# Performance work log

Measured on AMD Instinct MI355X. Metric: run time of the kernel, lower is better.

The kernel has to match this reference:

```python
import jax, jax.numpy as jnp
import numpy as np
from jax import lax

N_CHANNELS = 64
N_FILTERS = 256
N_LAYERS = 9  # residual blocks use dilations 2**1 .. 2**(N_LAYERS-1)


def causal_conv1d(x, w, dilation):
    """Causal dilated conv. x: [B,T,Cin], w: [K,Cin,Cout]."""
    pad = (w.shape[0] - 1) * dilation
    return lax.conv_general_dilated(
        x, w, window_strides=(1,), padding=[(pad, 0)],
        rhs_dilation=(dilation,), dimension_numbers=("NWC", "WIO", "NWC"))


def setup_inputs() -> dict:
    key = jax.random.key(0)
    ks = jax.random.split(key, 12)
    B, T, C, F, L = 8, 4096, N_CHANNELS, N_FILTERS, N_LAYERS
    s = lambda fan_in: 1.0 / np.sqrt(fan_in)
    return {
        "x": jax.random.normal(ks[0], (B, T, C), jnp.float32),
        "Wc": jax.random.normal(ks[1], (2, C, F), jnp.float32) * s(2 * C),
        "Wf": jax.random.normal(ks[2], (L - 1, 2, F, F), jnp.float32) * s(2 * F),
        "Wg": jax.random.normal(ks[3], (L - 1, 2, F, F), jnp.float32) * s(2 * F),
        "Wr": jax.random.normal(ks[4], (L - 1, F, F), jnp.float32) * s(F),
        "br": jnp.zeros((L - 1, F), jnp.float32),
        "Ws": jax.random.normal(ks[5], (L - 1, F, F), jnp.float32) * s(F),
        "bs": jnp.zeros((L - 1, F), jnp.float32),
        "Wd1": jax.random.normal(ks[6], (F, C), jnp.float32) * s(F),
        "bd1": jnp.zeros((C,), jnp.float32),
        "Wd2": jax.random.normal(ks[7], (C, C), jnp.float32) * s(C),
        "bd2": jnp.zeros((C,), jnp.float32),
    }


def reference(x, Wc, Wf, Wg, Wr, br, Ws, bs, Wd1, bd1, Wd2, bd2):
    # Initial causal conv, dilation 1, no bias.
    out = causal_conv1d(x, Wc, 1)  # [B,T,F]
    skip_sum = jnp.zeros_like(out)
    for i in range(N_LAYERS - 1):
        d = 2 ** (i + 1)
        f = causal_conv1d(out, Wf[i], d)
        g = causal_conv1d(out, Wg[i], d)
        z = jnp.tanh(f) * jax.nn.sigmoid(g)
        out = out + jnp.einsum("btf,fo->bto", z, Wr[i]) + br[i]
        skip_sum = skip_sum + jnp.einsum("btf,fo->bto", z, Ws[i]) + bs[i]
    h = jax.nn.selu(skip_sum)
    h = jnp.einsum("btf,fc->btc", h, Wd1) + bd1
    h = jax.nn.selu(h)
    h = jnp.einsum("btc,co->bto", h, Wd2) + bd2
    return h
```

## Files before the change

### kernel.cpp

```cpp
#include <hip/hip_runtime.h>
#include <cstdint>

typedef unsigned short u16;
typedef unsigned int u32;
typedef __attribute__((ext_vector_type(8))) short s8v;
typedef __attribute__((ext_vector_type(4))) float f4v;

#define FCH 256

__device__ __forceinline__ float bf2f(u16 u){ return __uint_as_float(((u32)u)<<16); }
__device__ __forceinline__ u16 f2bf(float x){
  u32 u = __float_as_uint(x);
  u += 0x7fffu + ((u>>16)&1u);
  return (u16)(u>>16);
}
__device__ __forceinline__ float rcpf(float x){ return __builtin_amdgcn_rcpf(x); }
__device__ __forceinline__ uint4 pack8(float4 a, float4 b){
  uint4 o;
  o.x = (u32)f2bf(a.x) | ((u32)f2bf(a.y)<<16);
  o.y = (u32)f2bf(a.z) | ((u32)f2bf(a.w)<<16);
  o.z = (u32)f2bf(b.x) | ((u32)f2bf(b.y)<<16);
  o.w = (u32)f2bf(b.z) | ((u32)f2bf(b.w)<<16);
  return o;
}
__device__ __forceinline__ float seluf(float x){
  const float sc = 1.0507009873554805f, al = 1.6732632423543772f;
  return x > 0.f ? sc*x : sc*al*(__expf(x)-1.f);
}
__device__ __forceinline__ s8v ldmask(const u16* p, u32 m){
  uint4 r = *reinterpret_cast<const uint4*>(p);
  r.x &= m; r.y &= m; r.z &= m; r.w &= m;
  s8v v; *reinterpret_cast<uint4*>(&v) = r;
  return v;
}
__device__ __forceinline__ int xcd_tile(int bid, int nT8){
  return nT8 ? ((bid & 7) * nT8 + (bid >> 3)) : bid;
}

__global__ __launch_bounds__(256) void pack_kernel(
    const float* __restrict__ Wc, const float* __restrict__ Wf, const float* __restrict__ Wg,
    const float* __restrict__ Wr, const float* __restrict__ Ws,
    const float* __restrict__ Wd1, const float* __restrict__ Wd2,
    u16* __restrict__ Bp1, u16* __restrict__ Bp2, u16* __restrict__ Bp0,
    u16* __restrict__ BpD1, u16* __restrict__ BpD2)
{
  int gid = blockIdx.x*256 + threadIdx.x;
  int frag = gid >> 6;
  int lane = gid & 63;
  int q = lane >> 4, i15 = lane & 15;
  u16 v[8];
  u16* dst;
  if (frag < 4096) {
    int layer = frag >> 9, rem = frag & 511;
    int kc = rem >> 5, nt = rem & 31;
    int n = nt*16 + i15;
    const float* W = (n < 256) ? Wf : Wg;
    int nn = (n < 256) ? n : n - 256;
    #pragma unroll
    for (int j = 0; j < 8; ++j) {
      int k = kc*32 + q*8 + j;
      int tap = k >> 8, cin = k & 255;
      v[j] = f2bf(W[((size_t)((layer*2 + tap)*256 + cin))*256 + nn]);
    }
    dst = Bp1 + (size_t)frag*512 + lane*8;
  } else if (frag < 6144) {
    int f = frag - 4096;
    int layer = f >> 8, rem = f & 255;
    int kc = rem >> 5, nt = rem & 31;
    int n = nt*16 + i15;
    const float* W = (n < 256) ? Wr : Ws;
    int nn = (n < 256) ? n : n - 256;
    #pragma unroll
    for (int j = 0; j < 8; ++j) {
      int k = kc*32 + q*8 + j;
      v[j] = f2bf(W[((size_t)(layer*256 + k))*256 + nn]);
    }
    dst = Bp2 + (size_t)f*512 + lane*8;
  } else if (frag < 6208) {
    int f = frag - 6144;
    int kc = f >> 4, nt = f & 15;
    int n = nt*16 + i15;
    #pragma unroll
    for (int j = 0; j < 8; ++j) {
      int k = kc*32 + q*8 + j;
      int tap = k >> 6, cin = k & 63;
      v[j] = f2bf(Wc[(size_t)(tap*64 + cin)*256 + n]);
    }
    dst = Bp0 + (size_t)f*512 + lane*8;
  } else if (frag < 6240) {
    int f = frag - 6208;
    int kc = f >> 2, nt = f & 3;
    int n = nt*16 + i15;
    #pragma unroll
    for (int j = 0; j < 8; ++j) {
      int k = kc*32 + q*8 + j;
      v[j] = f2bf(Wd1[(size_t)k*64 + n]);
    }
    dst = BpD1 + (size_t)f*512 + lane*8;
  } else if (frag < 6248) {
    int f = frag - 6240;
    int kc = f >> 2, nt = f & 3;
    int n = nt*16 + i15;
    #pragma unroll
    for (int j = 0; j < 8; ++j) {
      int k = kc*32 + q*8 + j;
      v[j] = f2bf(Wd2[(size_t)k*64 + n]);
    }
    dst = BpD2 + (size_t)f*512 + lane*8;
  } else return;
  uint4 o;
  o.x = (u32)v[0] | ((u32)v[1] << 16);
  o.y = (u32)v[2] | ((u32)v[3] << 16);
  o.z = (u32)v[4] | ((u32)v[5] << 16);
  o.w = (u32)v[6] | ((u32)v[7] << 16);
  *reinterpret_cast<uint4*>(dst) = o;
}

__global__ __launch_bounds__(256, 2) void conv0_kernel(
    const float* __restrict__ x, u16* __restrict__ outBf,
    const u16* __restrict__ Bp0, int nT8)
{
  __shared__ __align__(16) u16 ldsA[2][2048];
  const int tid = threadIdx.x;
  const int w = tid >> 6, lane = tid & 63, q = lane >> 4, i15 = lane & 15;
  const int rb = xcd_tile(blockIdx.x, nT8) * 64;
  const int sm = tid >> 2, sg = tid & 3;
  const int grow = rb + sm;
  const int tpos = grow & 4095;
  const int sunit = ((sm >> 4)*64 + sg*16 + ((sm & 15) ^ (sg << 1))) * 8;
  const int runit = (q*16 + (i15 ^ (q << 1))) * 8;

  f4v acc[4][4];
  #pragma unroll
  for (int jj = 0; jj < 4; ++jj)
    #pragma unroll
    for (int mt = 0; mt < 4; ++mt)
      acc[jj][mt] = (f4v){0.f,0.f,0.f,0.f};

  float4 f0 = {0.f,0.f,0.f,0.f}, f1 = {0.f,0.f,0.f,0.f};
  if (tpos >= 1) {
    const float* px = x + (size_t)(grow-1)*64 + sg*8;
    f0 = *reinterpret_cast<const float4*>(px);
    f1 = *reinterpret_cast<const float4*>(px + 4);
  }
  *reinterpret_cast<uint4*>(&ldsA[0][sunit]) = pack8(f0, f1);
  s8v bcur[4], bnxt[4];
  #pragma unroll
  for (int jj = 0; jj < 4; ++jj)
    bcur[jj] = *reinterpret_cast<const s8v*>(Bp0 + ((size_t)(w + 4*jj)*64 + lane)*8);
  __syncthreads();

  for (int kc = 0; kc < 4; ++kc) {
    const int cur = kc & 1;
    uint4 an = {0u,0u,0u,0u};
    if (kc < 3) {
      int kg = (kc+1)*32 + sg*8;
      int tap = kg >> 6, col = kg & 63;
      float4 g0 = {0.f,0.f,0.f,0.f}, g1 = {0.f,0.f,0.f,0.f};
      if (tap) {
        const float* px = x + (size_t)grow*64 + col;
        g0 = *reinterpret_cast<const float4*>(px);
        g1 = *reinterpret_cast<const float4*>(px + 4);
      } else if (tpos >= 1) {
        const float* px = x + (size_t)(grow-1)*64 + col;
        g0 = *reinterpret_cast<const float4*>(px);
        g1 = *reinterpret_cast<const float4*>(px + 4);
      }
      an = pack8(g0, g1);
      #pragma unroll
      for (int jj = 0; jj < 4; ++jj)
        bnxt[jj] = *reinterpret_cast<const s8v*>(Bp0 + (((size_t)(kc+1)*16 + (w + 4*jj))*64 + lane)*8);
    }
    s8v af[4];
    #pragma unroll
    for (int mt = 0; mt < 4; ++mt)
      af[mt] = *reinterpret_cast<const s8v*>(&ldsA[cur][mt*512 + runit]);
    #pragma unroll
    for (int jj = 0; jj < 4; ++jj)
      #pragma unroll
      for (int mt = 0; mt < 4; ++mt)
        acc[jj][mt] = __builtin_amdgcn_mfma_f32_16x16x32_bf16(af[mt], bcur[jj], acc[jj][mt], 0,0,0);
    if (kc < 3) {
      *reinterpret_cast<uint4*>(&ldsA[cur ^ 1][sunit]) = an;
      #pragma unroll
      for (int jj = 0; jj < 4; ++jj) bcur[jj] = bnxt[jj];
    }
    __syncthreads();
  }

  #pragma unroll
  for (int jj = 0; jj < 4; ++jj) {
    const int cc = (w + 4*jj)*16 + i15;
    #pragma unroll
    for (int mt = 0; mt < 4; ++mt)
      #pragma unroll
      for (int r = 0; r < 4; ++r) {
        const int g2 = rb + mt*16 + q*4 + r;
        outBf[(size_t)g2*FCH + cc] = f2bf(acc[jj][mt][r]);
      }
  }
}

__global__ __launch_bounds__(256, 3) void layer_kernel(
    const u16* __restrict__ inBf, u16* __restrict__ outBf,
    u16* __restrict__ skipB,
    const u16* __restrict__ Bp1, const u16* __restrict__ Bp2,
    const float* __restrict__ br, const float* __restrict__ bs,
    const u16* __restrict__ BpD1, const u16* __restrict__ BpD2,
    const float* __restrict__ bd1, const float* __restrict__ bd2,
    float* __restrict__ outp,
    int dil, int first, int last, int nT8)
{
  __shared__ __align__(16) u16 ldsZ[32*264];
  __shared__ __align__(16) u16 ldsH2[32*72];
  const int tid = threadIdx.x;
  const int w = __builtin_amdgcn_readfirstlane(tid >> 6);
  const int lane = tid & 63, q = lane >> 4, i15 = lane & 15;
  const int rb = xcd_tile(blockIdx.x, nT8) * 32;

  f4v acc[8][2];
  #pragma unroll
  for (int jj = 0; jj < 8; ++jj)
    #pragma unroll
    for (int mt = 0; mt < 2; ++mt)
      acc[jj][mt] = (f4v){0.f,0.f,0.f,0.f};

  {
    const u16* a0p[2];
    const u16* a1p[2];
    u32 am[2];
    #pragma unroll
    for (int mt = 0; mt < 2; ++mt) {
      const int row = rb + mt*16 + i15;
      const bool v = (row & 4095) >= dil;
      a0p[mt] = inBf + (size_t)(v ? row - dil : row)*FCH + q*8;
      a1p[mt] = inBf + (size_t)row*FCH + q*8;
      am[mt]  = v ? 0xffffffffu : 0u;
    }

    s8v bb[3][4], aa[4][2];
    #pragma unroll
    for (int j2 = 0; j2 < 4; ++j2) {
      bb[0][j2] = *reinterpret_cast<const s8v*>(Bp1 + ((size_t)(w + 4*j2)*64 + lane)*8);
      bb[1][j2] = *reinterpret_cast<const s8v*>(Bp1 + ((size_t)(w + 16 + 4*j2)*64 + lane)*8);
    }
    #pragma unroll
    for (int c = 0; c < 3; ++c)
      #pragma unroll
      for (int mt = 0; mt < 2; ++mt)
        aa[c][mt] = ldmask(a0p[mt] + c*32, am[mt]);

    #pragma unroll
    for (int s = 0; s < 32; ++s) {
      const int kc = s >> 1, h = s & 1;
      if (s + 2 < 32) {
        const int sp = s + 2, kcp = sp >> 1, hp = sp & 1;
        #pragma unroll
        for (int j2 = 0; j2 < 4; ++j2)
          bb[sp % 3][j2] = *reinterpret_cast<const s8v*>(
              Bp1 + (((size_t)kcp*32 + (w + 16*hp + 4*j2))*64 + lane)*8);
      }
      if (h == 0 && kc + 3 < 16) {
        const int ca = kc + 3;
        if (ca < 8) {
          #pragma unroll
          for (int mt = 0; mt < 2; ++mt)
            aa[ca & 3][mt] = ldmask(a0p[mt] + ca*32, am[mt]);
        } else {
          #pragma unroll
          for (int mt = 0; mt < 2; ++mt)
            aa[ca & 3][mt] = *reinterpret_cast<const s8v*>(a1p[mt] + (ca - 8)*32);
        }
      }
      __builtin_amdgcn_s_setprio(1);
      #pragma unroll
      for (int j2 = 0; j2 < 4; ++j2)
        #pragma unroll
        for (int mt = 0; mt < 2; ++mt)
          acc[h*4 + j2][mt] = __builtin_amdgcn_mfma_f32_16x16x32_bf16(
              aa[kc & 3][mt], bb[s % 3][j2], acc[h*4 + j2][mt], 0,0,0);
      __builtin_amdgcn_s_setprio(0);
    }
  }

  s8v s2b[3][4];
  #pragma unroll
  for (int j2 = 0; j2 < 4; ++j2) {
    s2b[0][j2] = *reinterpret_cast<const s8v*>(Bp2 + ((size_t)(w + 4*j2)*64 + lane)*8);
    s2b[1][j2] = *reinterpret_cast<const s8v*>(Bp2 + ((size_t)(w + 16 + 4*j2)*64 + lane)*8);
  }
  u16 skv[4][2][4];
  if (!first) {
    #pragma unroll
    for (int jj = 0; jj < 4; ++jj) {
      const int cc = (w + 4*jj)*16 + i15;
      #pragma unroll
      for (int mt = 0; mt < 2; ++mt)
        #pragma unroll
        for (int r = 0; r < 4; ++r)
          skv[jj][mt][r] = skipB[(size_t)(rb + mt*16 + q*4 + r)*FCH + cc];
    }
  }

  #pragma unroll
  for (int jj = 0; jj < 4; ++jj) {
    const int colb = (w + 4*jj)*16 + i15;
    #pragma unroll
    for (int mt = 0; mt < 2; ++mt)
      #pragma unroll
      for (int r = 0; r < 4; ++r) {
        float f = acc[jj][mt][r];
        float g = acc[jj+4][mt][r];
        float z = (1.f - 2.f*rcpf(__expf(2.f*f) + 1.f)) * rcpf(1.f + __expf(-g));
        ldsZ[(mt*16 + q*4 + r)*264 + colb] = f2bf(z);
      }
  }
  #pragma unroll
  for (int jj = 0; jj < 8; ++jj)
    #pragma unroll
    for (int mt = 0; mt < 2; ++mt)
      acc[jj][mt] = (f4v){0.f,0.f,0.f,0.f};
  __syncthreads();

  {
    s8v zf[2][2];
    #pragma unroll
    for (int mt = 0; mt < 2; ++mt)
      zf[0][mt] = *reinterpret_cast<const s8v*>(&ldsZ[(mt*16 + i15)*264 + q*8]);
    #pragma unroll
    for (int s = 0; s < 16; ++s) {
      const int kc = s >> 1, h = s & 1;
      if (s + 2 < 16) {
        const int sp = s + 2, kcp = sp >> 1, hp = sp & 1;
        #pragma unroll
        for (int j2 = 0; j2 < 4; ++j2)
          s2b[sp % 3][j2] = *reinterpret_cast<const s8v*>(
              Bp2 + (((size_t)kcp*32 + (w + 16*hp + 4*j2))*64 + lane)*8);
        if (hp == 0) {
          #pragma unroll
          for (int mt = 0; mt < 2; ++mt)
            zf[kcp & 1][mt] = *reinterpret_cast<const s8v*>(&ldsZ[(mt*16 + i15)*264 + kcp*32 + q*8]);
        }
      }
      __builtin_amdgcn_s_setprio(1);
      #pragma unroll
      for (int j2 = 0; j2 < 4; ++j2)
        #pragma unroll
        for (int mt = 0; mt < 2; ++mt)
          acc[h*4 + j2][mt] = __builtin_amdgcn_mfma_f32_16x16x32_bf16(
              zf[kc & 1][mt], s2b[s % 3][j2], acc[h*4 + j2][mt], 0,0,0);
      __builtin_amdgcn_s_setprio(0);
    }
  }

  if (!last) {
    u16 resv[4][2][4];
    #pragma unroll
    for (int jj = 0; jj < 4; ++jj) {
      const int cc = (w + 4*jj)*16 + i15;
      #pragma unroll
      for (int mt = 0; mt < 2; ++mt)
        #pragma unroll
        for (int r = 0; r < 4; ++r)
          resv[jj][mt][r] = inBf[(size_t)(rb + mt*16 + q*4 + r)*FCH + cc];
    }
    #pragma unroll
    for (int jj = 0; jj < 4; ++jj) {
      const int cc = (w + 4*jj)*16 + i15;
      const float bias = br[cc];
      #pragma unroll
      for (int mt = 0; mt < 2; ++mt)
        #pragma unroll
        for (int r = 0; r < 4; ++r) {
          const int g2 = rb + mt*16 + q*4 + r;
          float vv = acc[jj][mt][r] + bias + bf2f(resv[jj][mt][r]);
          outBf[(size_t)g2*FCH + cc] = f2bf(vv);
        }
    }
    #pragma unroll
    for (int jj = 4; jj < 8; ++jj) {
      const int cc = (jj - 4 + 0)*0 + ((w + 4*jj - 16 - 4*4 + 16))*0;
      const int cc2 = ((w + 4*jj) - 16)*16 + i15;
      const float bias = bs[cc2];
      #pragma unroll
      for (int mt = 0; mt < 2; ++mt)
        #pragma unroll
        for (int r = 0; r < 4; ++r) {
          const int g2 = rb + mt*16 + q*4 + r;
          float vv = acc[jj][mt][r] + bias;
          if (!first) vv += bf2f(skv[jj-4][mt][r]);
          skipB[(size_t)g2*FCH + cc2] = f2bf(vv);
        }
    }
    return;
  }

  __syncthreads();
  #pragma unroll
  for (int jj = 4; jj < 8; ++jj) {
    const int cc = ((w + 4*jj) - 16)*16 + i15;
    const float bias = bs[cc];
    #pragma unroll
    for (int mt = 0; mt < 2; ++mt)
      #pragma unroll
      for (int r = 0; r < 4; ++r) {
        float vv = acc[jj][mt][r] + bias;
        if (!first) vv += bf2f(skv[jj-4][mt][r]);
        ldsZ[(mt*16 + q*4 + r)*264 + cc] = f2bf(seluf(vv));
      }
  }
  __syncthreads();

  f4v a1[2];
  #pragma unroll
  for (int mt = 0; mt < 2; ++mt) a1[mt] = (f4v){0.f,0.f,0.f,0.f};
  for (int kc = 0; kc < 8; ++kc) {
    s8v b = *reinterpret_cast<const s8v*>(BpD1 + ((size_t)(kc*4 + w)*64 + lane)*8);
    #pragma unroll
    for (int mt = 0; mt < 2; ++mt) {
      s8v af = *reinterpret_cast<const s8v*>(&ldsZ[(mt*16 + i15)*264 + kc*32 + q*8]);
      a1[mt] = __builtin_amdgcn_mfma_f32_16x16x32_bf16(af, b, a1[mt], 0,0,0);
    }
  }
  const float bb1 = bd1[w*16 + i15];
  #pragma unroll
  for (int mt = 0; mt < 2; ++mt)
    #pragma unroll
    for (int r = 0; r < 4; ++r)
      ldsH2[(mt*16 + q*4 + r)*72 + w*16 + i15] = f2bf(seluf(a1[mt][r] + bb1));
  __syncthreads();

  f4v a2[2];
  #pragma unroll
  for (int mt = 0; mt < 2; ++mt) a2[mt] = (f4v){0.f,0.f,0.f,0.f};
  #pragma unroll
  for (int kc = 0; kc < 2; ++kc) {
    s8v b = *reinterpret_cast<const s8v*>(BpD2 + ((size_t)(kc*4 + w)*64 + lane)*8);
    #pragma unroll
    for (int mt = 0; mt < 2; ++mt) {
      s8v af = *reinterpret_cast<const s8v*>(&ldsH2[(mt*16 + i15)*72 + kc*32 + q*8]);
      a2[mt] = __builtin_amdgcn_mfma_f32_16x16x32_bf16(af, b, a2[mt], 0,0,0);
    }
  }
  const float bb2 = bd2[w*16 + i15];
  #pragma unroll
  for (int mt = 0; mt < 2; ++mt)
    #pragma unroll
    for (int r = 0; r < 4; ++r)
      outp[(size_t)(rb + mt*16 + q*4 + r)*64 + w*16 + i15] = a2[mt][r] + bb2;
}

__global__ __launch_bounds__(256) void zero_kernel(uint4* __restrict__ outp, int n16)
{
  int i = blockIdx.x*256 + threadIdx.x;
  if (i < n16) outp[i] = (uint4){0u,0u,0u,0u};
}

extern "C" void kernel_launch(void* const* d_in, const int* in_sizes, int n_in,
                              void* d_out, int out_size, void* d_ws, size_t ws_size,
                              hipStream_t stream)
{
  (void)n_in;
  const float* x   = (const float*)d_in[0];
  const float* Wc  = (const float*)d_in[1];
  const float* Wf  = (const float*)d_in[2];
  const float* Wg  = (const float*)d_in[3];
  const float* Wr  = (const float*)d_in[4];
  const float* br  = (const float*)d_in[5];
  const float* Ws  = (const float*)d_in[6];
  const float* bs  = (const float*)d_in[7];
  const float* Wd1 = (const float*)d_in[8];
  const float* bd1 = (const float*)d_in[9];
  const float* Wd2 = (const float*)d_in[10];
  const float* bd2 = (const float*)d_in[11];

  const size_t ROWS = (size_t)in_sizes[0] / 64;
  const int gridC = (int)(ROWS / 64);
  const int gridL = (int)(ROWS / 32);
  const int nT8C = (gridC % 8 == 0) ? gridC / 8 : 0;
  const int nT8L = (gridL % 8 == 0) ? gridL / 8 : 0;

  const size_t packsB = (size_t)6248 * 512 * 2;
  const size_t bfBuf  = ROWS * 256 * 2;
  const size_t needB = packsB + 3*bfBuf;

  if (ws_size < needB) {
    int n16 = (out_size * 4) / 16;
    zero_kernel<<<(n16 + 255)/256, 256, 0, stream>>>((uint4*)d_out, n16);
    return;
  }

  char* ws = (char*)d_ws;
  u16* Bp1    = (u16*)ws;            ws += (size_t)4096*512*2;
  u16* Bp2    = (u16*)ws;            ws += (size_t)2048*512*2;
  u16* Bp0    = (u16*)ws;            ws += (size_t)64*512*2;
  u16* BpD1   = (u16*)ws;            ws += (size_t)32*512*2;
  u16* BpD2   = (u16*)ws;            ws += (size_t)8*512*2;
  u16* skipB  = (u16*)ws;            ws += bfBuf;
  u16* bufA   = (u16*)ws;            ws += bfBuf;
  u16* bufB   = (u16*)ws;            ws += bfBuf;

  pack_kernel<<<1562, 256, 0, stream>>>(Wc, Wf, Wg, Wr, Ws, Wd1, Wd2,
                                        Bp1, Bp2, Bp0, BpD1, BpD2);
  conv0_kernel<<<gridC, 256, 0, stream>>>(x, bufA, Bp0, nT8C);
  u16* bufs[2] = {bufA, bufB};
  for (int i = 0; i < 8; ++i) {
    layer_kernel<<<gridL, 256, 0, stream>>>(
        bufs[i & 1], bufs[(i + 1) & 1], skipB,
        Bp1 + (size_t)i*262144, Bp2 + (size_t)i*131072,
        br + i*256, bs + i*256,
        BpD1, BpD2, bd1, bd2, (float*)d_out,
        2 << i, (i == 0) ? 1 : 0, (i == 7) ? 1 : 0, nT8L);
  }
}
```

Measured before the change: 520.1 us.

## Split gated and output GEMMs into halves to cut accumulators and raise occupancy

The layer kernel now computes the filter and gate GEMMs in two sequential passes, each with half the accumulators. The filter result is staged in LDS as packed bf16 between the passes. The residual and skip output GEMMs are likewise split into two passes, and the residual pass is skipped on the last layer. Together with launch bounds raised from 3 to 4 blocks, this aims to lower register pressure and increase occupancy. The cost is re-reading the A operand from global memory, extra LDS traffic and footprint, and an extra bf16 rounding of the filter pre-activation.

After: 623.2 us. +19.8%, slower.

```diff
diff --git a/kernel.cpp b/kernel.cpp
--- a/kernel.cpp
+++ b/kernel.cpp
@@ -201,7 +201,7 @@
   }
 }
 
-__global__ __launch_bounds__(256, 3) void layer_kernel(
+__global__ __launch_bounds__(256, 4) void layer_kernel(
     const u16* __restrict__ inBf, u16* __restrict__ outBf,
     u16* __restrict__ skipB,
     const u16* __restrict__ Bp1, const u16* __restrict__ Bp2,
@@ -212,202 +212,288 @@
     int dil, int first, int last, int nT8)
 {
   __shared__ __align__(16) u16 ldsZ[32*264];
+  __shared__ __align__(16) u32 ldsF[16*256];
   __shared__ __align__(16) u16 ldsH2[32*72];
   const int tid = threadIdx.x;
   const int w = __builtin_amdgcn_readfirstlane(tid >> 6);
   const int lane = tid & 63, q = lane >> 4, i15 = lane & 15;
   const int rb = xcd_tile(blockIdx.x, nT8) * 32;
 
-  f4v acc[8][2];
-  #pragma unroll
-  for (int jj = 0; jj < 8; ++jj)
+  u32 a0o[2], a1o[2], am[2];
+  #pragma unroll
+  for (int mt = 0; mt < 2; ++mt) {
+    const int row = rb + mt*16 + i15;
+    const bool v = (row & 4095) >= dil;
+    a0o[mt] = (u32)(v ? row - dil : row)*FCH + q*8;
+    a1o[mt] = (u32)row*FCH + q*8;
+    am[mt]  = v ? 0xffffffffu : 0u;
+  }
+
+  f4v acc[4][2];
+
+  #pragma unroll
+  for (int j = 0; j < 4; ++j)
     #pragma unroll
     for (int mt = 0; mt < 2; ++mt)
-      acc[jj][mt] = (f4v){0.f,0.f,0.f,0.f};
-
+      acc[j][mt] = (f4v){0.f,0.f,0.f,0.f};
   {
-    const u16* a0p[2];
-    const u16* a1p[2];
-    u32 am[2];
-    #pragma unroll
-    for (int mt = 0; mt < 2; ++mt) {
-      const int row = rb + mt*16 + i15;
-      const bool v = (row & 4095) >= dil;
-      a0p[mt] = inBf + (size_t)(v ? row - dil : row)*FCH + q*8;
-      a1p[mt] = inBf + (size_t)row*FCH + q*8;
-      am[mt]  = v ? 0xffffffffu : 0u;
-    }
-
-    s8v bb[3][4], aa[4][2];
-    #pragma unroll
-    for (int j2 = 0; j2 < 4; ++j2) {
-      bb[0][j2] = *reinterpret_cast<const s8v*>(Bp1 + ((size_t)(w + 4*j2)*64 + lane)*8);
-      bb[1][j2] = *reinterpret_cast<const s8v*>(Bp1 + ((size_t)(w + 16 + 4*j2)*64 + lane)*8);
-    }
-    #pragma unroll
-    for (int c = 0; c < 3; ++c)
+    s8v bb[3][4], aa[3][2];
+    #pragma unroll
+    for (int j = 0; j < 4; ++j) {
+      bb[0][j] = *reinterpret_cast<const s8v*>(Bp1 + ((size_t)(w + 4*j)*64 + lane)*8);
+      bb[1][j] = *reinterpret_cast<const s8v*>(Bp1 + ((size_t)(32 + w + 4*j)*64 + lane)*8);
+    }
+    #pragma unroll
+    for (int c = 0; c < 2; ++c)
       #pragma unroll
       for (int mt = 0; mt < 2; ++mt)
-        aa[c][mt] = ldmask(a0p[mt] + c*32, am[mt]);
-
-    #pragma unroll
-    for (int s = 0; s < 32; ++s) {
-      const int kc = s >> 1, h = s & 1;
-      if (s + 2 < 32) {
-        const int sp = s + 2, kcp = sp >> 1, hp = sp & 1;
-        #pragma unroll
-        for (int j2 = 0; j2 < 4; ++j2)
-          bb[sp % 3][j2] = *reinterpret_cast<const s8v*>(
-              Bp1 + (((size_t)kcp*32 + (w + 16*hp + 4*j2))*64 + lane)*8);
-      }
-      if (h == 0 && kc + 3 < 16) {
-        const int ca = kc + 3;
-        if (ca < 8) {
+        aa[c][mt] = ldmask(inBf + a0o[mt] + c*32, am[mt]);
+
+    #pragma unroll
+    for (int kc = 0; kc < 16; ++kc) {
+      if (kc + 2 < 16) {
+        const int kp = kc + 2;
+        #pragma unroll
+        for (int j = 0; j < 4; ++j)
+          bb[kp % 3][j] = *reinterpret_cast<const s8v*>(
+              Bp1 + (((size_t)kp*32 + w + 4*j)*64 + lane)*8);
+        if (kp < 8) {
           #pragma unroll
           for (int mt = 0; mt < 2; ++mt)
-            aa[ca & 3][mt] = ldmask(a0p[mt] + ca*32, am[mt]);
+            aa[kp % 3][mt] = ldmask(inBf + a0o[mt] + kp*32, am[mt]);
         } else {
           #pragma unroll
           for (int mt = 0; mt < 2; ++mt)
-            aa[ca & 3][mt] = *reinterpret_cast<const s8v*>(a1p[mt] + (ca - 8)*32);
+            aa[kp % 3][mt] = *reinterpret_cast<const s8v*>(inBf + a1o[mt] + (kp - 8)*32);
         }
       }
       __builtin_amdgcn_s_setprio(1);
       #pragma unroll
-      for (int j2 = 0; j2 < 4; ++j2)
+      for (int j = 0; j < 4; ++j)
         #pragma unroll
         for (int mt = 0; mt < 2; ++mt)
-          acc[h*4 + j2][mt] = __builtin_amdgcn_mfma_f32_16x16x32_bf16(
-              aa[kc & 3][mt], bb[s % 3][j2], acc[h*4 + j2][mt], 0,0,0);
+          acc[j][mt] = __builtin_amdgcn_mfma_f32_16x16x32_bf16(
+              aa[kc % 3][mt], bb[kc % 3][j], acc[j][mt], 0,0,0);
       __builtin_amdgcn_s_setprio(0);
     }
   }
-
-  s8v s2b[3][4];
-  #pragma unroll
-  for (int j2 = 0; j2 < 4; ++j2) {
-    s2b[0][j2] = *reinterpret_cast<const s8v*>(Bp2 + ((size_t)(w + 4*j2)*64 + lane)*8);
-    s2b[1][j2] = *reinterpret_cast<const s8v*>(Bp2 + ((size_t)(w + 16 + 4*j2)*64 + lane)*8);
-  }
-  u16 skv[4][2][4];
-  if (!first) {
-    #pragma unroll
-    for (int jj = 0; jj < 4; ++jj) {
-      const int cc = (w + 4*jj)*16 + i15;
-      #pragma unroll
-      for (int mt = 0; mt < 2; ++mt)
-        #pragma unroll
-        for (int r = 0; r < 4; ++r)
-          skv[jj][mt][r] = skipB[(size_t)(rb + mt*16 + q*4 + r)*FCH + cc];
-    }
-  }
-
-  #pragma unroll
-  for (int jj = 0; jj < 4; ++jj) {
-    const int colb = (w + 4*jj)*16 + i15;
+  #pragma unroll
+  for (int j = 0; j < 4; ++j)
+    #pragma unroll
+    for (int mt = 0; mt < 2; ++mt) {
+      ldsF[((j*2 + mt)*2 + 0)*256 + tid] =
+          (u32)f2bf(acc[j][mt][0]) | ((u32)f2bf(acc[j][mt][1]) << 16);
+      ldsF[((j*2 + mt)*2 + 1)*256 + tid] =
+          (u32)f2bf(acc[j][mt][2]) | ((u32)f2bf(acc[j][mt][3]) << 16);
+    }
+
+  #pragma unroll
+  for (int j = 0; j < 4; ++j)
     #pragma unroll
     for (int mt = 0; mt < 2; ++mt)
+      acc[j][mt] = (f4v){0.f,0.f,0.f,0.f};
+  {
+    s8v bb[3][4], aa[2][2];
+    #pragma unroll
+    for (int j = 0; j < 4; ++j) {
+      bb[0][j] = *reinterpret_cast<const s8v*>(Bp1 + ((size_t)(16 + w + 4*j)*64 + lane)*8);
+      bb[1][j] = *reinterpret_cast<const s8v*>(Bp1 + ((size_t)(32 + 16 + w + 4*j)*64 + lane)*8);
+    }
+    #pragma unroll
+    for (int mt = 0; mt < 2; ++mt)
+      aa[0][mt] = ldmask(inBf + a0o[mt], am[mt]);
+
+    #pragma unroll
+    for (int kc = 0; kc < 16; ++kc) {
+      if (kc + 2 < 16) {
+        const int kp = kc + 2;
+        #pragma unroll
+        for (int j = 0; j < 4; ++j)
+          bb[kp % 3][j] = *reinterpret_cast<const s8v*>(
+              Bp1 + (((size_t)kp*32 + 16 + w + 4*j)*64 + lane)*8);
+      }
+      if (kc + 1 < 16) {
+        const int kn = kc + 1;
+        if (kn < 8) {
+          #pragma unroll
+          for (int mt = 0; mt < 2; ++mt)
+            aa[kn & 1][mt] = ldmask(inBf + a0o[mt] + kn*32, am[mt]);
+        } else {
+          #pragma unroll
+          for (int mt = 0; mt < 2; ++mt)
+            aa[kn & 1][mt] = *reinterpret_cast<const s8v*>(inBf + a1o[mt] + (kn - 8)*32);
+        }
+      }
+      __builtin_amdgcn_s_setprio(1);
+      #pragma unroll
+      for (int j = 0; j < 4; ++j)
+        #pragma unroll
+        for (int mt = 0; mt < 2; ++mt)
+          acc[j][mt] = __builtin_amdgcn_mfma_f32_16x16x32_bf16(
+              aa[kc & 1][mt], bb[kc % 3][j], acc[j][mt], 0,0,0);
+      __builtin_amdgcn_s_setprio(0);
+    }
+  }
+
+  #pragma unroll
+  for (int j = 0; j < 4; ++j) {
+    const int colb = (w + 4*j)*16 + i15;
+    #pragma unroll
+    for (int mt = 0; mt < 2; ++mt) {
+      const u32 p0 = ldsF[((j*2 + mt)*2 + 0)*256 + tid];
+      const u32 p1 = ldsF[((j*2 + mt)*2 + 1)*256 + tid];
+      float fv[4] = { bf2f((u16)(p0 & 0xffffu)), bf2f((u16)(p0 >> 16)),
+                      bf2f((u16)(p1 & 0xffffu)), bf2f((u16)(p1 >> 16)) };
       #pragma unroll
       for (int r = 0; r < 4; ++r) {
-        float f = acc[jj][mt][r];
-        float g = acc[jj+4][mt][r];
+        float f = fv[r];
+        float g = acc[j][mt][r];
         float z = (1.f - 2.f*rcpf(__expf(2.f*f) + 1.f)) * rcpf(1.f + __expf(-g));
         ldsZ[(mt*16 + q*4 + r)*264 + colb] = f2bf(z);
       }
-  }
-  #pragma unroll
-  for (int jj = 0; jj < 8; ++jj)
+    }
+  }
+  __syncthreads();
+
+  if (!last) {
+    #pragma unroll
+    for (int j = 0; j < 4; ++j)
+      #pragma unroll
+      for (int mt = 0; mt < 2; ++mt)
+        acc[j][mt] = (f4v){0.f,0.f,0.f,0.f};
+    {
+      s8v bb[3][4], zf[2][2];
+      #pragma unroll
+      for (int j = 0; j < 4; ++j) {
+        bb[0][j] = *reinterpret_cast<const s8v*>(Bp2 + ((size_t)(w + 4*j)*64 + lane)*8);
+        bb[1][j] = *reinterpret_cast<const s8v*>(Bp2 + ((size_t)(32 + w + 4*j)*64 + lane)*8);
+      }
+      #pragma unroll
+      for (int mt = 0; mt < 2; ++mt)
+        zf[0][mt] = *reinterpret_cast<const s8v*>(&ldsZ[(mt*16 + i15)*264 + q*8]);
+      #pragma unroll
+      for (int kc = 0; kc < 8; ++kc) {
+        if (kc + 2 < 8) {
+          const int kp = kc + 2;
+          #pragma unroll
+          for (int j = 0; j < 4; ++j)
+            bb[kp % 3][j] = *reinterpret_cast<const s8v*>(
+                Bp2 + (((size_t)kp*32 + w + 4*j)*64 + lane)*8);
+        }
+        if (kc + 1 < 8) {
+          const int kn = kc + 1;
+          #pragma unroll
+          for (int mt = 0; mt < 2; ++mt)
+            zf[kn & 1][mt] = *reinterpret_cast<const s8v*>(&ldsZ[(mt*16 + i15)*264 + kn*32 + q*8]);
+        }
+        __builtin_amdgcn_s_setprio(1);
+        #pragma unroll
+        for (int j = 0; j < 4; ++j)
+          #pragma unroll
+          for (int mt = 0; mt < 2; ++mt)
+            acc[j][mt] = __builtin_amdgcn_mfma_f32_16x16x32_bf16(
+                zf[kc & 1][mt], bb[kc % 3][j], acc[j][mt], 0,0,0);
+        __builtin_amdgcn_s_setprio(0);
+      }
+    }
+    #pragma unroll
+    for (int j = 0; j < 4; ++j) {
+      const int cc = (w + 4*j)*16 + i15;
+      const float bias = br[cc];
+      #pragma unroll
+      for (int mt = 0; mt < 2; ++mt)
+        #pragma unroll
+        for (int r = 0; r < 4; ++r) {
+          const int g2 = rb + mt*16 + q*4 + r;
+          float vv = acc[j][mt][r] + bias + bf2f(inBf[(size_t)g2*FCH + cc]);
+          outBf[(size_t)g2*FCH + cc] = f2bf(vv);
+        }
+    }
+  }
+
+  #pragma unroll
+  for (int j = 0; j < 4; ++j)
     #pragma unroll
     for (int mt = 0; mt < 2; ++mt)
-      acc[jj][mt] = (f4v){0.f,0.f,0.f,0.f};
-  __syncthreads();
-
+      acc[j][mt] = (f4v){0.f,0.f,0.f,0.f};
   {
-    s8v zf[2][2];
+    s8v bb[3][4], zf[2][2];
+    #pragma unroll
+    for (int j = 0; j < 4; ++j) {
+      bb[0][j] = *reinterpret_cast<const s8v*>(Bp2 + ((size_t)(16 + w + 4*j)*64 + lane)*8);
+      bb[1][j] = *reinterpret_cast<const s8v*>(Bp2 + ((size_t)(32 + 16 + w + 4*j)*64 + lane)*8);
+    }
     #pragma unroll
     for (int mt = 0; mt < 2; ++mt)
       zf[0][mt] = *reinterpret_cast<const s8v*>(&ldsZ[(mt*16 + i15)*264 + q*8]);
     #pragma unroll
-    for (int s = 0; s < 16; ++s) {
-      const int kc = s >> 1, h = s & 1;
-      if (s + 2 < 16) {
-        const int sp = s + 2, kcp = sp >> 1, hp = sp & 1;
-        #pragma unroll
-        for (int j2 = 0; j2 < 4; ++j2)
-          s2b[sp % 3][j2] = *reinterpret_cast<const s8v*>(
-              Bp2 + (((size_t)kcp*32 + (w + 16*hp + 4*j2))*64 + lane)*8);
-        if (hp == 0) {
-          #pragma unroll
-          for (int mt = 0; mt < 2; ++mt)
-            zf[kcp & 1][mt] = *reinterpret_cast<const s8v*>(&ldsZ[(mt*16 + i15)*264 + kcp*32 + q*8]);
-        }
+    for (int kc = 0; kc < 8; ++kc) {
+      if (kc + 2 < 8) {
+        const int kp = kc + 2;
+        #pragma unroll
+        for (int j = 0; j < 4; ++j)
+          bb[kp % 3][j] = *reinterpret_cast<const s8v*>(
+              Bp2 + (((size_t)kp*32 + 16 + w + 4*j)*64 + lane)*8);
+      }
+      if (kc + 1 < 8) {
+        const int kn = kc + 1;
+        #pragma unroll
+        for (int mt = 0; mt < 2; ++mt)
+          zf[kn & 1][mt] = *reinterpret_cast<const s8v*>(&ldsZ[(mt*16 + i15)*264 + kn*32 + q*8]);
       }
       __builtin_amdgcn_s_setprio(1);
       #pragma unroll
-      for (int j2 = 0; j2 < 4; ++j2)
+      for (int j = 0; j < 4; ++j)
         #pragma unroll
         for (int mt = 0; mt < 2; ++mt)
-          acc[h*4 + j2][mt] = __builtin_amdgcn_mfma_f32_16x16x32_bf16(
-              zf[kc & 1][mt], s2b[s % 3][j2], acc[h*4 + j2][mt], 0,0,0);
+          acc[j][mt] = __builtin_amdgcn_mfma_f32_16x16x32_bf16(
+              zf[kc & 1][mt], bb[kc % 3][j], acc[j][mt], 0,0,0);
       __builtin_amdgcn_s_setprio(0);
     }
   }
 
   if (!last) {
-    u16 resv[4][2][4];
-    #pragma unroll
-    for (int jj = 0; jj < 4; ++jj) {
-      const int cc = (w + 4*jj)*16 + i15;
-      #pragma unroll
-      for (int mt = 0; mt < 2; ++mt)
-        #pragma unroll
-        for (int r = 0; r < 4; ++r)
-          resv[jj][mt][r] = inBf[(size_t)(rb + mt*16 + q*4 + r)*FCH + cc];
-    }
-    #pragma unroll
-    for (int jj = 0; jj < 4; ++jj) {
-      const int cc = (w + 4*jj)*16 + i15;
-      const float bias = br[cc];
+    #pragma unroll
+    for (int j = 0; j < 4; ++j) {
+      const int cc = (w + 4*j)*16 + i15;
+      const float bias = bs[cc];
       #pragma unroll
       for (int mt = 0; mt < 2; ++mt)
         #pragma unroll
         for (int r = 0; r < 4; ++r) {
           const int g2 = rb + mt*16 + q*4 + r;
-          float vv = acc[jj][mt][r] + bias + bf2f(resv[jj][mt][r]);
-          outBf[(size_t)g2*FCH + cc] = f2bf(vv);
+          float vv = acc[j][mt][r] + bias;
+          if (!first) vv += bf2f(skipB[(size_t)g2*FCH + cc]);
+          skipB[(size_t)g2*FCH + cc] = f2bf(vv);
         }
     }
-    #pragma unroll
-    for (int jj = 4; jj < 8; ++jj) {
-      const int cc = (jj - 4 + 0)*0 + ((w + 4*jj - 16 - 4*4 + 16))*0;
-      const int cc2 = ((w + 4*jj) - 16)*16 + i15;
-      const float bias = bs[cc2];
+    return;
+  }
+
+  {
+    u16 skv[4][2][4];
+    #pragma unroll
+    for (int j = 0; j < 4; ++j) {
+      const int cc = (w + 4*j)*16 + i15;
       #pragma unroll
       for (int mt = 0; mt < 2; ++mt)
         #pragma unroll
+        for (int r = 0; r < 4; ++r)
+          skv[j][mt][r] = skipB[(size_t)(rb + mt*16 + q*4 + r)*FCH + cc];
+    }
+    __syncthreads();
+    #pragma unroll
+    for (int j = 0; j < 4; ++j) {
+      const int cc = (w + 4*j)*16 + i15;
+      const float bias = bs[cc];
+      #pragma unroll
+      for (int mt = 0; mt < 2; ++mt)
+        #pragma unroll
         for (int r = 0; r < 4; ++r) {
-          const int g2 = rb + mt*16 + q*4 + r;
-          float vv = acc[jj][mt][r] + bias;
-          if (!first) vv += bf2f(skv[jj-4][mt][r]);
-          skipB[(size_t)g2*FCH + cc2] = f2bf(vv);
+          float vv = acc[j][mt][r] + bias + bf2f(skv[j][mt][r]);
+          ldsZ[(mt*16 + q*4 + r)*264 + cc] = f2bf(seluf(vv));
         }
     }
-    return;
-  }
-
-  __syncthreads();
-  #pragma unroll
-  for (int jj = 4; jj < 8; ++jj) {
-    const int cc = ((w + 4*jj) - 16)*16 + i15;
-    const float bias = bs[cc];
-    #pragma unroll
-    for (int mt = 0; mt < 2; ++mt)
-      #pragma unroll
-      for (int r = 0; r < 4; ++r) {
-        float vv = acc[jj][mt][r] + bias;
-        if (!first) vv += bf2f(skv[jj-4][mt][r]);
-        ldsZ[(mt*16 + q*4 + r)*264 + cc] = f2bf(seluf(vv));
-      }
   }
   __syncthreads();
 
```
